# Kernel tuning notes

Hardware: AMD Instinct MI355X
Metric: run time of the kernel (lower is better)

The kernel has to match this reference:

```python
import jax, jax.numpy as jnp
import numpy as np

B, S, D, H = 4, 2048, 1024, 16
HD = D // H  # head dim = 64


def setup_inputs() -> dict:
    key = jax.random.key(0)
    ks = jax.random.split(key, 6)
    hidden_states = jax.random.normal(ks[0], (B, S, D), dtype=jnp.float32)
    attention_mask = jnp.zeros((B, S), dtype=bool)  # ignored by the module (set to None in forward)
    # RoPE cache: standard rotary angles per position
    inv_freq = 1.0 / (10000.0 ** (jnp.arange(0, HD, 2, dtype=jnp.float32) / HD))  # [HD/2]
    ang = jnp.arange(S, dtype=jnp.float32)[:, None] * inv_freq[None, :]  # [S, HD/2]
    ang = jnp.concatenate([ang, ang], axis=-1)  # [S, HD]
    rope_cos = jnp.cos(ang)
    rope_sin = jnp.sin(ang)
    scale = 1.0 / np.sqrt(D)
    Wq = jax.random.normal(ks[1], (D, D), dtype=jnp.float32) * scale
    Wk = jax.random.normal(ks[2], (D, D), dtype=jnp.float32) * scale
    Wv = jax.random.normal(ks[3], (D, D), dtype=jnp.float32) * scale
    return {"hidden_states": hidden_states, "attention_mask": attention_mask,
            "rope_cos": rope_cos, "rope_sin": rope_sin, "Wq": Wq, "Wk": Wk, "Wv": Wv}


def _rotate_half(x):
    x1, x2 = jnp.split(x, 2, axis=-1)
    return jnp.concatenate([-x2, x1], axis=-1)


def _apply_rope(x, cos, sin):
    # x: [B, H, S, HD]; cos/sin: [S, HD]
    return x * cos[None, None, :, :] + _rotate_half(x) * sin[None, None, :, :]


def reference(hidden_states, attention_mask, rope_cos, rope_sin, Wq, Wk, Wv):
    del attention_mask  # forward() sets attention_mask = None
    b, s, d = hidden_states.shape
    # QKV projections (nn.Linear: y = x @ W.T), split into heads -> [B, H, S, HD]
    def proj(W):
        y = jnp.einsum('bsd,ed->bse', hidden_states, W)
        return y.reshape(b, s, H, HD).transpose(0, 2, 1, 3)
    q = _apply_rope(proj(Wq), rope_cos, rope_sin)
    k = _apply_rope(proj(Wk), rope_cos, rope_sin)
    v = proj(Wv)
    # Softmax attention (non-causal, dropout_p=0)
    scores = jnp.einsum('bhqd,bhkd->bhqk', q, k) / np.sqrt(HD)
    probs = jax.nn.softmax(scores, axis=-1)
    ctx = jnp.einsum('bhqk,bhkd->bhqd', probs, v)
    # [B, H, S, HD] -> [B, S, D]
    return ctx.transpose(0, 2, 1, 3).reshape(b, s, d)
```

## Files before the change

### kernel.cpp

```cpp
#include <hip/hip_runtime.h>
#include <hip/hip_bf16.h>
#include <stdint.h>


typedef __attribute__((ext_vector_type(4))) float    f32x4;
typedef __attribute__((ext_vector_type(8))) __bf16   bf16x8;
typedef __attribute__((ext_vector_type(8))) unsigned short ushort8;
typedef __attribute__((ext_vector_type(4))) unsigned short ushort4v;

#define QSCALE 0.18033688011112042f
#define SMAX   16.0f

#define GLOAD_LDS16(g, l)                                                     \
  __builtin_amdgcn_global_load_lds(                                           \
      (const __attribute__((address_space(1))) void*)(g),                     \
      (__attribute__((address_space(3))) void*)(l), 16, 0, 0)

__device__ inline unsigned short bf(float f) {
  return __builtin_bit_cast(unsigned short, (__bf16)f);
}

__global__ __launch_bounds__(256) void cvt_bf16(
    const float* __restrict__ X,
    const float* __restrict__ Wq, const float* __restrict__ Wk,
    const float* __restrict__ Wv,
    unsigned short* __restrict__ Xb, unsigned short* __restrict__ Wb)
{
  const int seg = blockIdx.y;
  const float* __restrict__ src = (seg == 0) ? X : (seg == 1) ? Wq : (seg == 2) ? Wk : Wv;
  unsigned short* __restrict__ dst = (seg == 0) ? Xb : Wb + (size_t)(seg - 1) * 1048576;
  const size_t n8 = (seg == 0) ? (size_t)1048576 : (size_t)131072;
  const size_t stride = (size_t)gridDim.x * 256;
  for (size_t i = blockIdx.x * 256 + threadIdx.x; i < n8; i += stride) {
    const float4 a = *reinterpret_cast<const float4*>(src + i * 8);
    const float4 b = *reinterpret_cast<const float4*>(src + i * 8 + 4);
    ushort8 o = { bf(a.x), bf(a.y), bf(a.z), bf(a.w), bf(b.x), bf(b.y), bf(b.z), bf(b.w) };
    *reinterpret_cast<ushort8*>(dst + i * 8) = o;
  }
}

__global__ __launch_bounds__(256) void qkv_gemm(
    const unsigned short* __restrict__ Xb, const unsigned short* __restrict__ Wb,
    const float* __restrict__ rc, const float* __restrict__ rs,
    unsigned short* __restrict__ Qb, unsigned short* __restrict__ Kb,
    unsigned short* __restrict__ VbT, int col0, int nheads_c, int gx)
{
  const int nwg = gridDim.x;
  const int q8 = nwg >> 3;
  int w = (blockIdx.x % 8) * q8 + blockIdx.x / 8;
  const int z = w / (gx * 64);
  const int r = w - z * gx * 64;
  const int brow = (r / gx) * 128;
  const int bcol = (r % gx) * 128;

  const unsigned short* __restrict__ Wz = Wb + (size_t)z * 1048576;

  const int tid  = threadIdx.x;
  const int lane = tid & 63;
  const int wid  = tid >> 6;
  const int wm = wid >> 1, wn = wid & 1;
  const int col16 = lane & 15, rowg = lane >> 4;

  __shared__ unsigned short As[128 * 32];
  __shared__ unsigned short Bs[128 * 32];

  f32x4 acc[4][4];
  #pragma unroll
  for (int m = 0; m < 4; ++m)
    #pragma unroll
    for (int n = 0; n < 4; ++n) acc[m][n] = (f32x4)0.f;

  const int srow = wid * 16 + (lane >> 2);
  const int scol = (lane & 3) * 8;
  const unsigned short* gA0 = Xb + (size_t)(brow + srow) * 1024 + scol;
  const unsigned short* gA1 = gA0 + (size_t)64 * 1024;
  const unsigned short* gB0 = Wz + (size_t)(col0 + bcol + srow) * 1024 + scol;
  const unsigned short* gB1 = gB0 + (size_t)64 * 1024;
  unsigned short* lA0 = &As[wid * 16 * 32];
  unsigned short* lA1 = &As[(64 + wid * 16) * 32];
  unsigned short* lB0 = &Bs[wid * 16 * 32];
  unsigned short* lB1 = &Bs[(64 + wid * 16) * 32];

  for (int k0 = 0; k0 < 1024; k0 += 32) {
    GLOAD_LDS16(gA0 + k0, lA0);
    GLOAD_LDS16(gA1 + k0, lA1);
    GLOAD_LDS16(gB0 + k0, lB0);
    GLOAD_LDS16(gB1 + k0, lB1);
    __syncthreads();

    bf16x8 af[4], bfv[4];
    #pragma unroll
    for (int m = 0; m < 4; ++m)
      af[m] = __builtin_bit_cast(bf16x8, *reinterpret_cast<const ushort8*>(
                &As[(wm * 64 + m * 16 + col16) * 32 + rowg * 8]));
    #pragma unroll
    for (int n = 0; n < 4; ++n)
      bfv[n] = __builtin_bit_cast(bf16x8, *reinterpret_cast<const ushort8*>(
                &Bs[(wn * 64 + n * 16 + col16) * 32 + rowg * 8]));
    #pragma unroll
    for (int m = 0; m < 4; ++m)
      #pragma unroll
      for (int n = 0; n < 4; ++n)
        acc[m][n] = __builtin_amdgcn_mfma_f32_16x16x32_bf16(af[m], bfv[n], acc[m][n], 0, 0, 0);
    __syncthreads();
  }

  #pragma unroll
  for (int m = 0; m < 4; ++m) {
    #pragma unroll
    for (int n = 0; n < 4; ++n) {
      const int e  = bcol + wn * 64 + n * 16 + col16;
      const int hl = e >> 6, hd = e & 63;
      if (z == 2) {
        const int row0 = brow + wm * 64 + m * 16 + rowg * 4;
        const int b = row0 >> 11, s0 = row0 & 2047;
        ushort4v o = { bf(acc[m][n][0]), bf(acc[m][n][1]), bf(acc[m][n][2]), bf(acc[m][n][3]) };
        *reinterpret_cast<ushort4v*>(
            VbT + ((size_t)(b * nheads_c + hl) * 64 + hd) * 2048 + s0) = o;
      } else {
        unsigned short* __restrict__ outp = (z == 0) ? Qb : Kb;
        #pragma unroll
        for (int j = 0; j < 4; ++j) {
          const int row = brow + wm * 64 + m * 16 + rowg * 4 + j;
          const int b = row >> 11, s = row & 2047;
          const float rot = (n < 2) ? -acc[m][n + 2][j] : acc[m][n - 2][j];
          float v = acc[m][n][j] * rc[s * 64 + hd] + rot * rs[s * 64 + hd];
          if (z == 0) v *= QSCALE;
          outp[((size_t)(b * nheads_c + hl) * 2048 + s) * 64 + hd] = bf(v);
        }
      }
    }
  }
}

__global__ __launch_bounds__(256) void attn(
    const unsigned short* __restrict__ Qb, const unsigned short* __restrict__ Kb,
    const unsigned short* __restrict__ VbT, float* __restrict__ out,
    int col0, int nheads_c)
{
  const int tid = threadIdx.x, lane = tid & 63, wq = tid >> 6;
  const int col16 = lane & 15, rowg = lane >> 4;

  int wg = blockIdx.x;
  const int qx = (int)gridDim.x >> 3;
  wg = (wg & 7) * qx + (wg >> 3);
  const int bh = wg >> 4;
  const int q0 = (wg & 15) * 128;
  const int b = bh / nheads_c, hl = bh - b * nheads_c;
  const int hg = (col0 >> 6) + hl;
  const size_t base = (size_t)bh * 2048 * 64;

  __shared__ unsigned short Ks[64 * 72];
  __shared__ unsigned short Vt[64 * 72];
  __shared__ unsigned short Ps[128 * 76];

  const int r  = tid >> 3, c  = (tid & 7) * 8;
  const int vr = tid >> 2, vc = (tid & 3) * 16;

  #pragma unroll
  for (int p = 0; p < 4; ++p) {
    const int row = p * 32 + r;
    ushort8 v = *reinterpret_cast<const ushort8*>(Qb + base + (size_t)(q0 + row) * 64 + c);
    *reinterpret_cast<ushort8*>(&Ps[row * 76 + c]) = v;
  }
  __syncthreads();
  bf16x8 qf[2][2];
  #pragma unroll
  for (int m = 0; m < 2; ++m)
    #pragma unroll
    for (int ks = 0; ks < 2; ++ks)
      qf[m][ks] = __builtin_bit_cast(bf16x8, *reinterpret_cast<const ushort8*>(
          &Ps[(wq * 32 + m * 16 + col16) * 76 + ks * 32 + rowg * 8]));

  float lsum[2][4];
  f32x4 acc[2][4];
  #pragma unroll
  for (int m = 0; m < 2; ++m)
    #pragma unroll
    for (int j = 0; j < 4; ++j) lsum[m][j] = 0.f;
  #pragma unroll
  for (int m = 0; m < 2; ++m)
    #pragma unroll
    for (int hf = 0; hf < 4; ++hf) acc[m][hf] = (f32x4)0.f;

  for (int kt = 0; kt < 32; ++kt) {
    const int key0 = kt * 64;
    {
      ushort8 k0 = *reinterpret_cast<const ushort8*>(Kb + base + (size_t)(key0 + r) * 64 + c);
      ushort8 k1 = *reinterpret_cast<const ushort8*>(Kb + base + (size_t)(key0 + 32 + r) * 64 + c);
      ushort8 v0 = *reinterpret_cast<const ushort8*>(VbT + base + (size_t)vr * 2048 + key0 + vc);
      ushort8 v1 = *reinterpret_cast<const ushort8*>(VbT + base + (size_t)vr * 2048 + key0 + vc + 8);
      *reinterpret_cast<ushort8*>(&Ks[r * 72 + c]) = k0;
      *reinterpret_cast<ushort8*>(&Ks[(32 + r) * 72 + c]) = k1;
      *reinterpret_cast<ushort8*>(&Vt[vr * 72 + vc]) = v0;
      *reinterpret_cast<ushort8*>(&Vt[vr * 72 + vc + 8]) = v1;
    }
    __syncthreads();

    f32x4 sc[2][4];
    #pragma unroll
    for (int m = 0; m < 2; ++m)
      #pragma unroll
      for (int kf = 0; kf < 4; ++kf) sc[m][kf] = (f32x4)0.f;
    #pragma unroll
    for (int kf = 0; kf < 4; ++kf) {
      #pragma unroll
      for (int ks = 0; ks < 2; ++ks) {
        bf16x8 kfrag = __builtin_bit_cast(bf16x8, *reinterpret_cast<const ushort8*>(
            &Ks[(kf * 16 + col16) * 72 + ks * 32 + rowg * 8]));
        sc[0][kf] = __builtin_amdgcn_mfma_f32_16x16x32_bf16(qf[0][ks], kfrag, sc[0][kf], 0, 0, 0);
        sc[1][kf] = __builtin_amdgcn_mfma_f32_16x16x32_bf16(qf[1][ks], kfrag, sc[1][kf], 0, 0, 0);
      }
    }

    #pragma unroll
    for (int m = 0; m < 2; ++m)
      #pragma unroll
      for (int j = 0; j < 4; ++j) {
        float ps = 0.f;
        #pragma unroll
        for (int kf = 0; kf < 4; ++kf) {
          const float p = __builtin_exp2f(sc[m][kf][j] - SMAX);
          sc[m][kf][j] = p;
          ps += p;
        }
        lsum[m][j] += ps;
      }

    #pragma unroll
    for (int m = 0; m < 2; ++m)
      #pragma unroll
      for (int kf = 0; kf < 4; ++kf)
        #pragma unroll
        for (int j = 0; j < 4; ++j)
          Ps[(wq * 32 + m * 16 + rowg * 4 + j) * 76 + kf * 16 + col16] = bf(sc[m][kf][j]);
    __syncthreads();

    #pragma unroll
    for (int ks = 0; ks < 2; ++ks) {
      bf16x8 pf[2];
      #pragma unroll
      for (int m = 0; m < 2; ++m)
        pf[m] = __builtin_bit_cast(bf16x8, *reinterpret_cast<const ushort8*>(
            &Ps[(wq * 32 + m * 16 + col16) * 76 + ks * 32 + rowg * 8]));
      #pragma unroll
      for (int hf = 0; hf < 4; ++hf) {
        bf16x8 vf = __builtin_bit_cast(bf16x8, *reinterpret_cast<const ushort8*>(
            &Vt[(hf * 16 + col16) * 72 + ks * 32 + rowg * 8]));
        acc[0][hf] = __builtin_amdgcn_mfma_f32_16x16x32_bf16(pf[0], vf, acc[0][hf], 0, 0, 0);
        acc[1][hf] = __builtin_amdgcn_mfma_f32_16x16x32_bf16(pf[1], vf, acc[1][hf], 0, 0, 0);
      }
    }
    __syncthreads();
  }

  #pragma unroll
  for (int m = 0; m < 2; ++m)
    #pragma unroll
    for (int j = 0; j < 4; ++j) {
      float l = lsum[m][j];
      l += __shfl_xor(l, 1);
      l += __shfl_xor(l, 2);
      l += __shfl_xor(l, 4);
      l += __shfl_xor(l, 8);
      const float inv = 1.0f / l;
      const int s = q0 + wq * 32 + m * 16 + rowg * 4 + j;
      #pragma unroll
      for (int hf = 0; hf < 4; ++hf) {
        const int hd = hf * 16 + col16;
        out[((size_t)(b * 2048 + s)) * 1024 + hg * 64 + hd] = acc[m][hf][j] * inv;
      }
    }
}

extern "C" void kernel_launch(void* const* d_in, const int* in_sizes, int n_in,
                              void* d_out, int out_size, void* d_ws, size_t ws_size,
                              hipStream_t stream) {
  (void)in_sizes; (void)n_in; (void)out_size;
  const float* X  = (const float*)d_in[0];
  const float* rc = (const float*)d_in[2];
  const float* rs = (const float*)d_in[3];
  const float* Wq = (const float*)d_in[4];
  const float* Wk = (const float*)d_in[5];
  const float* Wv = (const float*)d_in[6];
  float* out = (float*)d_out;

  const size_t fixed = (size_t)2 * 8192 * 1024 + (size_t)3 * 2 * 1024 * 1024;
  int NC = 8;
  for (int nc = 1; nc <= 8; nc <<= 1) {
    size_t need = (size_t)3 * 2 * 8192 * (1024 / nc) + fixed;
    if (need <= ws_size) { NC = nc; break; }
  }
  const int CW = 1024 / NC;
  const int nheads_c = CW >> 6;
  const int nBH = 4 * nheads_c;
  const int gx = CW / 128;
  const size_t pc = (size_t)8192 * CW;

  unsigned short* Qb  = (unsigned short*)d_ws;
  unsigned short* Kb  = Qb + pc;
  unsigned short* VbT = Kb + pc;
  unsigned short* Xb  = VbT + pc;
  unsigned short* Wb  = Xb + (size_t)8192 * 1024;

  cvt_bf16<<<dim3(512, 4), 256, 0, stream>>>(X, Wq, Wk, Wv, Xb, Wb);

  for (int c = 0; c < NC; ++c) {
    const int col0 = c * CW;
    qkv_gemm<<<dim3(gx * 64 * 3), 256, 0, stream>>>(
        Xb, Wb, rc, rs, Qb, Kb, VbT, col0, nheads_c, gx);
    attn<<<dim3(16 * nBH), 256, 0, stream>>>(
        Qb, Kb, VbT, out, col0, nheads_c);
  }
}
```

Before: 206.2 us.

## Split attention query tile across eight waves of sixteen rows each

The attention kernel now runs 512 threads per block, with each of eight waves owning 16 query rows instead of four waves owning 32. Per-thread K/V staging drops to one 16-byte load each, and each wave keeps half the score and accumulator fragments. The aim is more waves to hide latency and fewer registers per wave. The cost is that each K/V fragment read from LDS feeds fewer MFMAs, and barriers now synchronise more waves. The GEMM macro is only renamed.

Measured after the change: 220.2 us. +6.8%, slower.

```diff
diff --git a/kernel.cpp b/kernel.cpp
--- a/kernel.cpp
+++ b/kernel.cpp
@@ -11,7 +11,7 @@
 #define QSCALE 0.18033688011112042f
 #define SMAX   16.0f
 
-#define GLOAD_LDS16(g, l)                                                     \
+#define GL16(g, l)                                                            \
   __builtin_amdgcn_global_load_lds(                                           \
       (const __attribute__((address_space(1))) void*)(g),                     \
       (__attribute__((address_space(3))) void*)(l), 16, 0, 0)
@@ -82,10 +82,10 @@
   unsigned short* lB1 = &Bs[(64 + wid * 16) * 32];
 
   for (int k0 = 0; k0 < 1024; k0 += 32) {
-    GLOAD_LDS16(gA0 + k0, lA0);
-    GLOAD_LDS16(gA1 + k0, lA1);
-    GLOAD_LDS16(gB0 + k0, lB0);
-    GLOAD_LDS16(gB1 + k0, lB1);
+    GL16(gA0 + k0, lA0);
+    GL16(gA1 + k0, lA1);
+    GL16(gB0 + k0, lB0);
+    GL16(gB1 + k0, lB1);
     __syncthreads();
 
     bf16x8 af[4], bfv[4];
@@ -133,7 +133,7 @@
   }
 }
 
-__global__ __launch_bounds__(256) void attn(
+__global__ __launch_bounds__(512) void attn(
     const unsigned short* __restrict__ Qb, const unsigned short* __restrict__ Kb,
     const unsigned short* __restrict__ VbT, float* __restrict__ out,
     int col0, int nheads_c)
@@ -154,123 +154,97 @@
   __shared__ unsigned short Vt[64 * 72];
   __shared__ unsigned short Ps[128 * 76];
 
-  const int r  = tid >> 3, c  = (tid & 7) * 8;
-  const int vr = tid >> 2, vc = (tid & 3) * 16;
-
-  #pragma unroll
-  for (int p = 0; p < 4; ++p) {
-    const int row = p * 32 + r;
-    ushort8 v = *reinterpret_cast<const ushort8*>(Qb + base + (size_t)(q0 + row) * 64 + c);
-    *reinterpret_cast<ushort8*>(&Ps[row * 76 + c]) = v;
+  const int sr = tid >> 3, sc8 = (tid & 7) * 8;
+
+  #pragma unroll
+  for (int p = 0; p < 2; ++p) {
+    const int row = p * 64 + sr;
+    ushort8 v = *reinterpret_cast<const ushort8*>(Qb + base + (size_t)(q0 + row) * 64 + sc8);
+    *reinterpret_cast<ushort8*>(&Ps[row * 76 + sc8]) = v;
   }
   __syncthreads();
-  bf16x8 qf[2][2];
-  #pragma unroll
-  for (int m = 0; m < 2; ++m)
-    #pragma unroll
-    for (int ks = 0; ks < 2; ++ks)
-      qf[m][ks] = __builtin_bit_cast(bf16x8, *reinterpret_cast<const ushort8*>(
-          &Ps[(wq * 32 + m * 16 + col16) * 76 + ks * 32 + rowg * 8]));
-
-  float lsum[2][4];
-  f32x4 acc[2][4];
-  #pragma unroll
-  for (int m = 0; m < 2; ++m)
-    #pragma unroll
-    for (int j = 0; j < 4; ++j) lsum[m][j] = 0.f;
-  #pragma unroll
-  for (int m = 0; m < 2; ++m)
-    #pragma unroll
-    for (int hf = 0; hf < 4; ++hf) acc[m][hf] = (f32x4)0.f;
+  bf16x8 qf[2];
+  #pragma unroll
+  for (int ks = 0; ks < 2; ++ks)
+    qf[ks] = __builtin_bit_cast(bf16x8, *reinterpret_cast<const ushort8*>(
+        &Ps[(wq * 16 + col16) * 76 + ks * 32 + rowg * 8]));
+
+  float lsum[4] = {0.f, 0.f, 0.f, 0.f};
+  f32x4 acc[4];
+  #pragma unroll
+  for (int hf = 0; hf < 4; ++hf) acc[hf] = (f32x4)0.f;
 
   for (int kt = 0; kt < 32; ++kt) {
     const int key0 = kt * 64;
     {
-      ushort8 k0 = *reinterpret_cast<const ushort8*>(Kb + base + (size_t)(key0 + r) * 64 + c);
-      ushort8 k1 = *reinterpret_cast<const ushort8*>(Kb + base + (size_t)(key0 + 32 + r) * 64 + c);
-      ushort8 v0 = *reinterpret_cast<const ushort8*>(VbT + base + (size_t)vr * 2048 + key0 + vc);
-      ushort8 v1 = *reinterpret_cast<const ushort8*>(VbT + base + (size_t)vr * 2048 + key0 + vc + 8);
-      *reinterpret_cast<ushort8*>(&Ks[r * 72 + c]) = k0;
-      *reinterpret_cast<ushort8*>(&Ks[(32 + r) * 72 + c]) = k1;
-      *reinterpret_cast<ushort8*>(&Vt[vr * 72 + vc]) = v0;
-      *reinterpret_cast<ushort8*>(&Vt[vr * 72 + vc + 8]) = v1;
-    }
-    __syncthreads();
-
-    f32x4 sc[2][4];
-    #pragma unroll
-    for (int m = 0; m < 2; ++m)
-      #pragma unroll
-      for (int kf = 0; kf < 4; ++kf) sc[m][kf] = (f32x4)0.f;
+      ushort8 kv = *reinterpret_cast<const ushort8*>(Kb + base + (size_t)(key0 + sr) * 64 + sc8);
+      ushort8 vv = *reinterpret_cast<const ushort8*>(VbT + base + (size_t)sr * 2048 + key0 + sc8);
+      *reinterpret_cast<ushort8*>(&Ks[sr * 72 + sc8]) = kv;
+      *reinterpret_cast<ushort8*>(&Vt[sr * 72 + sc8]) = vv;
+    }
+    __syncthreads();
+
+    f32x4 sc[4];
+    #pragma unroll
+    for (int kf = 0; kf < 4; ++kf) sc[kf] = (f32x4)0.f;
     #pragma unroll
     for (int kf = 0; kf < 4; ++kf) {
       #pragma unroll
       for (int ks = 0; ks < 2; ++ks) {
         bf16x8 kfrag = __builtin_bit_cast(bf16x8, *reinterpret_cast<const ushort8*>(
             &Ks[(kf * 16 + col16) * 72 + ks * 32 + rowg * 8]));
-        sc[0][kf] = __builtin_amdgcn_mfma_f32_16x16x32_bf16(qf[0][ks], kfrag, sc[0][kf], 0, 0, 0);
-        sc[1][kf] = __builtin_amdgcn_mfma_f32_16x16x32_bf16(qf[1][ks], kfrag, sc[1][kf], 0, 0, 0);
-      }
-    }
-
-    #pragma unroll
-    for (int m = 0; m < 2; ++m)
-      #pragma unroll
-      for (int j = 0; j < 4; ++j) {
-        float ps = 0.f;
-        #pragma unroll
-        for (int kf = 0; kf < 4; ++kf) {
-          const float p = __builtin_exp2f(sc[m][kf][j] - SMAX);
-          sc[m][kf][j] = p;
-          ps += p;
-        }
-        lsum[m][j] += ps;
-      }
-
-    #pragma unroll
-    for (int m = 0; m < 2; ++m)
-      #pragma unroll
-      for (int kf = 0; kf < 4; ++kf)
-        #pragma unroll
-        for (int j = 0; j < 4; ++j)
-          Ps[(wq * 32 + m * 16 + rowg * 4 + j) * 76 + kf * 16 + col16] = bf(sc[m][kf][j]);
+        sc[kf] = __builtin_amdgcn_mfma_f32_16x16x32_bf16(qf[ks], kfrag, sc[kf], 0, 0, 0);
+      }
+    }
+
+    #pragma unroll
+    for (int j = 0; j < 4; ++j) {
+      float ps = 0.f;
+      #pragma unroll
+      for (int kf = 0; kf < 4; ++kf) {
+        const float p = __builtin_exp2f(sc[kf][j] - SMAX);
+        sc[kf][j] = p;
+        ps += p;
+      }
+      lsum[j] += ps;
+    }
+
+    #pragma unroll
+    for (int kf = 0; kf < 4; ++kf)
+      #pragma unroll
+      for (int j = 0; j < 4; ++j)
+        Ps[(wq * 16 + rowg * 4 + j) * 76 + kf * 16 + col16] = bf(sc[kf][j]);
     __syncthreads();
 
     #pragma unroll
     for (int ks = 0; ks < 2; ++ks) {
-      bf16x8 pf[2];
-      #pragma unroll
-      for (int m = 0; m < 2; ++m)
-        pf[m] = __builtin_bit_cast(bf16x8, *reinterpret_cast<const ushort8*>(
-            &Ps[(wq * 32 + m * 16 + col16) * 76 + ks * 32 + rowg * 8]));
+      bf16x8 pf = __builtin_bit_cast(bf16x8, *reinterpret_cast<const ushort8*>(
+          &Ps[(wq * 16 + col16) * 76 + ks * 32 + rowg * 8]));
       #pragma unroll
       for (int hf = 0; hf < 4; ++hf) {
         bf16x8 vf = __builtin_bit_cast(bf16x8, *reinterpret_cast<const ushort8*>(
             &Vt[(hf * 16 + col16) * 72 + ks * 32 + rowg * 8]));
-        acc[0][hf] = __builtin_amdgcn_mfma_f32_16x16x32_bf16(pf[0], vf, acc[0][hf], 0, 0, 0);
-        acc[1][hf] = __builtin_amdgcn_mfma_f32_16x16x32_bf16(pf[1], vf, acc[1][hf], 0, 0, 0);
-      }
-    }
-    __syncthreads();
-  }
-
-  #pragma unroll
-  for (int m = 0; m < 2; ++m)
-    #pragma unroll
-    for (int j = 0; j < 4; ++j) {
-      float l = lsum[m][j];
-      l += __shfl_xor(l, 1);
-      l += __shfl_xor(l, 2);
-      l += __shfl_xor(l, 4);
-      l += __shfl_xor(l, 8);
-      const float inv = 1.0f / l;
-      const int s = q0 + wq * 32 + m * 16 + rowg * 4 + j;
-      #pragma unroll
-      for (int hf = 0; hf < 4; ++hf) {
-        const int hd = hf * 16 + col16;
-        out[((size_t)(b * 2048 + s)) * 1024 + hg * 64 + hd] = acc[m][hf][j] * inv;
-      }
-    }
+        acc[hf] = __builtin_amdgcn_mfma_f32_16x16x32_bf16(pf, vf, acc[hf], 0, 0, 0);
+      }
+    }
+    __syncthreads();
+  }
+
+  #pragma unroll
+  for (int j = 0; j < 4; ++j) {
+    float l = lsum[j];
+    l += __shfl_xor(l, 1);
+    l += __shfl_xor(l, 2);
+    l += __shfl_xor(l, 4);
+    l += __shfl_xor(l, 8);
+    const float inv = 1.0f / l;
+    const int s = q0 + wq * 16 + rowg * 4 + j;
+    #pragma unroll
+    for (int hf = 0; hf < 4; ++hf) {
+      const int hd = hf * 16 + col16;
+      out[((size_t)(b * 2048 + s)) * 1024 + hg * 64 + hd] = acc[hf][j] * inv;
+    }
+  }
 }
 
 extern "C" void kernel_launch(void* const* d_in, const int* in_sizes, int n_in,
@@ -309,7 +283,7 @@
     const int col0 = c * CW;
     qkv_gemm<<<dim3(gx * 64 * 3), 256, 0, stream>>>(
         Xb, Wb, rc, rs, Qb, Kb, VbT, col0, nheads_c, gx);
-    attn<<<dim3(16 * nBH), 256, 0, stream>>>(
+    attn<<<dim3(16 * nBH), 512, 0, stream>>>(
         Qb, Kb, VbT, out, col0, nheads_c);
   }
 }
```
